# Kernel optimization log

Hardware: AMD Instinct MI355X
Metric: run time of the kernel (lower is better)

## Reference

```python
import jax, jax.numpy as jnp
import numpy as np

DIM = 512
H = 48
W = 48
WS = 6
NH = 16
HEAD = DIM // NH
SCALE = HEAD ** -0.5
MLP_RATIO = 4
EPS = 1e-3  # keras LayerNormalization default epsilon
B = 16
L = H * W
M = WS * WS
NW = (H // WS) * (W // WS)


def _rel_pos_index(ws):
    # replicates tf.meshgrid (indexing='xy') construction exactly
    ch = np.arange(ws)
    cw = np.arange(ws)
    coords = np.stack(np.meshgrid(ch, cw))              # (2, ws, ws)
    cf = coords.reshape(2, -1)                          # (2, M)
    cf1 = np.concatenate([cf, np.zeros((2, 1), cf.dtype)], axis=1)  # (2, M+1) with global (0,0)
    rel = cf[:, :, None] - cf1[:, None, :]              # (2, M, M+1)
    rel = rel.transpose(1, 2, 0).copy()
    rel[:, :, 0] += ws - 1
    rel[:, :, 1] += ws - 1
    rel[:, :, 0] *= 2 * ws - 1
    return rel.sum(-1)                                  # (M, M+1)

REL_IDX = jnp.asarray(_rel_pos_index(WS))


def layernorm(x, g, b):
    m = x.mean(-1, keepdims=True)
    v = ((x - m) ** 2).mean(-1, keepdims=True)
    return (x - m) / jnp.sqrt(v + EPS) * g + b


def setup_inputs() -> dict:
    key = jax.random.key(0)
    ks = jax.random.split(key, 8)
    dense = lambda k, i, o: jax.random.normal(k, (i, o), jnp.float32) * (1.0 / np.sqrt(i))
    return dict(
        x=jax.random.normal(ks[0], (B, L, DIM), jnp.float32),
        xavg=jax.random.normal(ks[1], (B, 1, DIM), jnp.float32),
        w_kv=dense(ks[2], DIM, 2 * DIM), b_kv=jnp.zeros((2 * DIM,), jnp.float32),
        w_q=dense(ks[3], DIM, DIM), b_q=jnp.zeros((DIM,), jnp.float32),
        rel_bias_table=jax.random.normal(ks[4], ((2 * WS - 1) ** 2, NH), jnp.float32) * 0.02,
        g1=jnp.ones((DIM,), jnp.float32), be1=jnp.zeros((DIM,), jnp.float32),
        g2=jnp.ones((DIM,), jnp.float32), be2=jnp.zeros((DIM,), jnp.float32),
        w_fc1=dense(ks[5], DIM, MLP_RATIO * DIM), b_fc1=jnp.zeros((MLP_RATIO * DIM,), jnp.float32),
        w_fc2=dense(ks[6], MLP_RATIO * DIM, DIM), b_fc2=jnp.zeros((DIM,), jnp.float32),
    )


def _heads(t):
    # (B*, N, C) -> (B*, NH, N, HEAD)
    return t.reshape(t.shape[0], t.shape[1], NH, HEAD).transpose(0, 2, 1, 3)


def _forward(x, xavg, w_kv, b_kv, w_q, b_q, rel_bias_table, g1, be1, g2, be2,
             w_fc1, b_fc1, w_fc2, b_fc2):
    shortcut, shortcut_avg = x, xavg
    xn = layernorm(x, g1, be1)                          # (B, L, C)
    xavgn = layernorm(xavg, g1, be1)                    # (B, 1, C)

    # window partition: (B, L, C) -> (B*NW, M, C)
    xw = xn.reshape(B, H // WS, WS, W // WS, WS, DIM)
    xw = xw.transpose(0, 1, 3, 2, 4, 5).reshape(B * NW, M, DIM)

    # per-window tokens + repeated global token as keys/values
    xavgR = jnp.repeat(xavgn, NW, axis=0)               # (B*NW, 1, C), batch-major like tf.repeat
    x_c = jnp.concatenate([xw, xavgR], axis=1)          # (B*NW, M+1, C)

    kv = x_c @ w_kv + b_kv                              # (B*NW, M+1, 2C)
    q = xw @ w_q + b_q                                  # (B*NW, M, C)
    q_avg = xavgn @ w_q + b_q                           # (B, 1, C)
    kv_g = xn @ w_kv + b_kv                             # (B, L, 2C)

    k, v = jnp.split(kv, 2, axis=-1)
    kg, vg = jnp.split(kv_g, 2, axis=-1)

    qh = _heads(q) * SCALE                              # (B*NW, NH, M, HEAD)
    attn = jnp.einsum('bhqd,bhkd->bhqk', qh, _heads(k))  # (B*NW, NH, M, M+1)
    bias = rel_bias_table[REL_IDX.reshape(-1)].reshape(M, M + 1, NH)
    attn = attn + bias.transpose(2, 0, 1)[None]
    attn = jax.nn.softmax(attn, axis=-1)
    xo = jnp.einsum('bhqk,bhkd->bhqd', attn, _heads(v))
    xo = xo.transpose(0, 2, 1, 3).reshape(B * NW, M, DIM)

    # global token attends to all tokens
    qg = _heads(q_avg) * SCALE                          # (B, NH, 1, HEAD)
    attng = jax.nn.softmax(jnp.einsum('bhqd,bhkd->bhqk', qg, _heads(kg)), axis=-1)
    xavg_o = jnp.einsum('bhqk,bhkd->bhqd', attng, _heads(vg))
    xavg_o = xavg_o.transpose(0, 2, 1, 3).reshape(B, 1, DIM)

    # window reverse: (B*NW, M, C) -> (B, L, C)
    xr = xo.reshape(B, H // WS, W // WS, WS, WS, DIM)
    xr = xr.transpose(0, 1, 3, 2, 4, 5).reshape(B, L, DIM)

    x = shortcut + xr
    xavg = shortcut_avg + xavg_o

    mlp = lambda t: jax.nn.gelu(t @ w_fc1 + b_fc1, approximate=False) @ w_fc2 + b_fc2
    x = x + mlp(layernorm(x, g2, be2))
    xavg = xavg + mlp(layernorm(xavg, g2, be2))
    return x, xavg


def reference(x, xavg, w_kv, b_kv, w_q, b_q, rel_bias_table, g1, be1, g2, be2,
              w_fc1, b_fc1, w_fc2, b_fc2):
    return _forward(x, xavg, w_kv, b_kv, w_q, b_q, rel_bias_table, g1, be1, g2, be2,
                    w_fc1, b_fc1, w_fc2, b_fc2)
```

## Files before the change

### kernel.cpp

```cpp
#include <hip/hip_runtime.h>
#include <stdint.h>

#define DIM 512
#define NHEAD 16
#define HEADD 32
#define BATCH 16
#define SEQL 2304
#define XROWS (BATCH*SEQL)
#define NROWS (XROWS + BATCH)
#define ATT_SCALE 0.17677669529663687f

typedef __attribute__((ext_vector_type(8))) short short8;
typedef __attribute__((ext_vector_type(4))) float f32x4;

__device__ __forceinline__ float bf2f(unsigned short v) {
    union { unsigned u; float f; } t; t.u = ((unsigned)v) << 16; return t.f;
}
__device__ __forceinline__ unsigned short f2bf(float f) {
    union { float f; unsigned u; } t; t.f = f;
    unsigned r = t.u + 0x7fffu + ((t.u >> 16) & 1u);
    return (unsigned short)(r >> 16);
}
__device__ __forceinline__ void unpack8(const int4 c, float* o) {
    union { unsigned u; float f; } t;
    unsigned w0 = (unsigned)c.x, w1 = (unsigned)c.y, w2 = (unsigned)c.z, w3 = (unsigned)c.w;
    t.u = w0 << 16;         o[0] = t.f;
    t.u = w0 & 0xffff0000u; o[1] = t.f;
    t.u = w1 << 16;         o[2] = t.f;
    t.u = w1 & 0xffff0000u; o[3] = t.f;
    t.u = w2 << 16;         o[4] = t.f;
    t.u = w2 & 0xffff0000u; o[5] = t.f;
    t.u = w3 << 16;         o[6] = t.f;
    t.u = w3 & 0xffff0000u; o[7] = t.f;
}
__device__ __forceinline__ void gl_lds16(const void* g, void* l) {
    __builtin_amdgcn_global_load_lds((const __attribute__((address_space(1))) unsigned int*)g,
                                     (__attribute__((address_space(3))) unsigned int*)l,
                                     16, 0, 0);
}

__device__ __forceinline__ float gelu_exact(float v) {
    union { float f; unsigned u; } zc; zc.f = v * 0.70710678118654752f;
    unsigned sgn = zc.u & 0x80000000u;
    union { float f; unsigned u; } az; az.u = zc.u & 0x7fffffffu;
    float t  = __builtin_amdgcn_rcpf(fmaf(0.3275911f, az.f, 1.0f));
    float p  = t * fmaf(t, fmaf(t, fmaf(t, fmaf(t, 1.061405429f, -1.453152027f),
                                        1.421413741f), -0.284496736f), 0.254829592f);
    float e  = __expf(-az.f * az.f);
    union { float f; unsigned u; } er; er.f = fmaf(-p, e, 1.0f);
    er.u |= sgn;
    return 0.5f * v * (1.0f + er.f);
}

__device__ __forceinline__ void ln_row(const float* __restrict__ src, int lane,
                                       const float* __restrict__ g, const float* __restrict__ be,
                                       unsigned short* __restrict__ outrow) {
    int c0 = lane * 8;
    float4 v0 = *(const float4*)(src + c0);
    float4 v1 = *(const float4*)(src + c0 + 4);
    float s = v0.x+v0.y+v0.z+v0.w + v1.x+v1.y+v1.z+v1.w;
    float q = v0.x*v0.x+v0.y*v0.y+v0.z*v0.z+v0.w*v0.w + v1.x*v1.x+v1.y*v1.y+v1.z*v1.z+v1.w*v1.w;
    for (int m = 1; m < 64; m <<= 1) { s += __shfl_xor(s, m); q += __shfl_xor(q, m); }
    float mean = s * (1.0f/512.0f);
    float var  = q * (1.0f/512.0f) - mean*mean;
    float rs = rsqrtf(var + 1e-3f);
    float4 g0 = *(const float4*)(g + c0);
    float4 g1 = *(const float4*)(g + c0 + 4);
    float4 b0 = *(const float4*)(be + c0);
    float4 b1 = *(const float4*)(be + c0 + 4);
    unsigned short o[8];
    o[0] = f2bf((v0.x-mean)*rs*g0.x + b0.x);
    o[1] = f2bf((v0.y-mean)*rs*g0.y + b0.y);
    o[2] = f2bf((v0.z-mean)*rs*g0.z + b0.z);
    o[3] = f2bf((v0.w-mean)*rs*g0.w + b0.w);
    o[4] = f2bf((v1.x-mean)*rs*g1.x + b1.x);
    o[5] = f2bf((v1.y-mean)*rs*g1.y + b1.y);
    o[6] = f2bf((v1.z-mean)*rs*g1.z + b1.z);
    o[7] = f2bf((v1.w-mean)*rs*g1.w + b1.w);
    *(int4*)(outrow + c0) = *(const int4*)o;
}

#define TPOSE_BLKS 2816
#define SPACK_BLKS 90
#define LN1_BLKS   9220
__global__ __launch_bounds__(256) void prep_kernel(const float* __restrict__ w_q,
                                                   const float* __restrict__ w_kv,
                                                   const float* __restrict__ w_fc1,
                                                   const float* __restrict__ w_fc2,
                                                   unsigned short* __restrict__ Wqkv_t,
                                                   unsigned short* __restrict__ Wfc1_t,
                                                   unsigned short* __restrict__ Wfc2_t,
                                                   const float* __restrict__ b_q,
                                                   const float* __restrict__ b_kv,
                                                   const float* __restrict__ rel_table,
                                                   float* __restrict__ bqkv,
                                                   float* __restrict__ bias_exp,
                                                   const float* __restrict__ x,
                                                   const float* __restrict__ xavg,
                                                   const float* __restrict__ g1,
                                                   const float* __restrict__ be1,
                                                   unsigned short* __restrict__ xn) {
    __shared__ float tile[32][33];
    int blk = blockIdx.x;
    if (blk < TPOSE_BLKS) {
        int t = blk;
        const float* src; unsigned short* dst;
        int Kd, Nd, rowOff, tk;
        if (t < 256)        { src = w_q;   dst = Wqkv_t; Kd = 512;  Nd = 512;  rowOff = 0;   tk = 16; }
        else if (t < 768)   { t -= 256;  src = w_kv;  dst = Wqkv_t; Kd = 512;  Nd = 1024; rowOff = 512; tk = 16; }
        else if (t < 1792)  { t -= 768;  src = w_fc1; dst = Wfc1_t; Kd = 512;  Nd = 2048; rowOff = 0;   tk = 16; }
        else                { t -= 1792; src = w_fc2; dst = Wfc2_t; Kd = 2048; Nd = 512;  rowOff = 0;   tk = 64; }
        int k0 = (t % tk) * 32;
        int n0 = (t / tk) * 32;
        int tx = threadIdx.x & 31, ty = threadIdx.x >> 5;
        #pragma unroll
        for (int r = 0; r < 32; r += 8)
            tile[r + ty][tx] = src[(long)(k0 + r + ty) * Nd + n0 + tx];
        __syncthreads();
        #pragma unroll
        for (int r = 0; r < 32; r += 8)
            dst[(long)(rowOff + n0 + r + ty) * Kd + k0 + tx] = f2bf(tile[tx][r + ty]);
        return;
    }
    blk -= TPOSE_BLKS;
    if (blk < SPACK_BLKS) {
        int i = blk * 256 + threadIdx.x;
        if (i < 1536) { bqkv[i] = (i < 512) ? b_q[i] : b_kv[i - 512]; return; }
        i -= 1536;
        if (i < NHEAD*36*37) {
            int h = i / (36*37); int rem = i % (36*37); int qi = rem / 37; int j = rem % 37;
            int c0m = qi % 6, c1m = qi / 6;
            int c0n = (j < 36) ? (j % 6) : 0;
            int c1n = (j < 36) ? (j / 6) : 0;
            int id = (c0m - c0n + 5) * 11 + (c1m - c1n + 5);
            bias_exp[i] = rel_table[id * NHEAD + h];
        }
        return;
    }
    blk -= SPACK_BLKS;
    int wv = threadIdx.x >> 6, lane = threadIdx.x & 63;
    int r = blk * 4 + wv;
    if (r >= NROWS) return;
    const float* src = (r < XROWS) ? (x + (long)r * DIM) : (xavg + (long)(r - XROWS) * DIM);
    ln_row(src, lane, g1, be1, xn + (long)r * DIM);
}

__global__ __launch_bounds__(256) void ln_kernel(const float* __restrict__ p1,
                                                 const float* __restrict__ g, const float* __restrict__ be,
                                                 unsigned short* __restrict__ out, int nrows) {
    int wv = threadIdx.x >> 6, lane = threadIdx.x & 63;
    int r = blockIdx.x * 4 + wv;
    if (r >= nrows) return;
    ln_row(p1 + (long)r * DIM, lane, g, be, out + (long)r * DIM);
}

template<bool GELU_ACT, bool OUT_BF16, bool HAS_RES>
__global__ __launch_bounds__(256) void gemm_kernel(const short* __restrict__ A,
                                                   const short* __restrict__ Bt,
                                                   const float* __restrict__ bias,
                                                   void* __restrict__ Cout,
                                                   const float* __restrict__ Res,
                                                   int M, int N, int K, int nbx) {
    __shared__ short lds_a[128 * 64];
    __shared__ short lds_b[128 * 64];
    const int tid = threadIdx.x;
    const int lane = tid & 63;
    const int wv = tid >> 6;

    const int nwg = gridDim.x;
    const int orig = blockIdx.x;
    const int q = nwg >> 3, r = nwg & 7;
    const int xcd = orig & 7, lid = orig >> 3;
    const int wg = (xcd < r ? xcd * (q + 1) : r * (q + 1) + (xcd - r) * q) + lid;
    const int m0 = (wg / nbx) * 128;
    const int n0 = (wg % nbx) * 128;
    const int wm = (wv >> 1) * 64;
    const int wn = (wv & 1) * 64;

    f32x4 acc[4][4];
    #pragma unroll
    for (int i = 0; i < 4; i++)
        #pragma unroll
        for (int j = 0; j < 4; j++) { acc[i][j][0]=0.f; acc[i][j][1]=0.f; acc[i][j][2]=0.f; acc[i][j][3]=0.f; }

    const int srow = tid >> 3;
    const int msl  = (tid & 7) ^ (srow & 7);
    const short* Aa = A + (long)(m0 + srow) * K + msl * 8;
    const short* Bb = Bt + (long)(n0 + srow) * K + msl * 8;
    short* la = lds_a + tid * 8;
    short* lb = lds_b + tid * 8;

    const int quad = lane >> 4;
    const int l15 = lane & 15;
    const short* ra0 = lds_a + (wm + l15) * 64 + ((quad)     ^ (l15 & 7)) * 8;
    const short* ra1 = lds_a + (wm + l15) * 64 + ((4 + quad) ^ (l15 & 7)) * 8;
    const short* rb0 = lds_b + (wn + l15) * 64 + ((quad)     ^ (l15 & 7)) * 8;
    const short* rb1 = lds_b + (wn + l15) * 64 + ((4 + quad) ^ (l15 & 7)) * 8;

    for (int k0 = 0; k0 < K; k0 += 64) {
        __syncthreads();
        #pragma unroll
        for (int i = 0; i < 4; i++) {
            gl_lds16(Aa + (long)(i * 32) * K + k0, la + i * 256 * 8);
            gl_lds16(Bb + (long)(i * 32) * K + k0, lb + i * 256 * 8);
        }
        __syncthreads();
        short8 af[4], bf4[4];
        #pragma unroll
        for (int mt = 0; mt < 4; mt++) af[mt] = *(const short8*)(ra0 + mt * 16 * 64);
        #pragma unroll
        for (int nt = 0; nt < 4; nt++) bf4[nt] = *(const short8*)(rb0 + nt * 16 * 64);
        #pragma unroll
        for (int mt = 0; mt < 4; mt++)
            #pragma unroll
            for (int nt = 0; nt < 4; nt++)
                acc[mt][nt] = __builtin_amdgcn_mfma_f32_16x16x32_bf16(af[mt], bf4[nt], acc[mt][nt], 0, 0, 0);
        #pragma unroll
        for (int mt = 0; mt < 4; mt++) af[mt] = *(const short8*)(ra1 + mt * 16 * 64);
        #pragma unroll
        for (int nt = 0; nt < 4; nt++) bf4[nt] = *(const short8*)(rb1 + nt * 16 * 64);
        #pragma unroll
        for (int mt = 0; mt < 4; mt++)
            #pragma unroll
            for (int nt = 0; nt < 4; nt++)
                acc[mt][nt] = __builtin_amdgcn_mfma_f32_16x16x32_bf16(af[mt], bf4[nt], acc[mt][nt], 0, 0, 0);
    }

    #pragma unroll
    for (int mt = 0; mt < 4; mt++) {
        int rbase = m0 + wm + mt * 16 + quad * 4;
        #pragma unroll
        for (int nt = 0; nt < 4; nt++) {
            int col = n0 + wn + nt * 16 + l15;
            float bv = bias[col];
            #pragma unroll
            for (int r2 = 0; r2 < 4; r2++) {
                int row = rbase + r2;
                if (row < M) {
                    float v = acc[mt][nt][r2] + bv;
                    if (GELU_ACT) v = gelu_exact(v);
                    if (HAS_RES) v += Res[(long)row * N + col];
                    if (OUT_BF16) ((unsigned short*)Cout)[(long)row * N + col] = f2bf(v);
                    else          ((float*)Cout)[(long)row * N + col] = v;
                }
            }
        }
    }
}

__global__ __launch_bounds__(256) void attn_kernel(const short* __restrict__ qkv,
                                                   const float* __restrict__ bias_exp,
                                                   const float* __restrict__ xin,
                                                   const float* __restrict__ xavg,
                                                   float* __restrict__ XALL) {
    __shared__ short vt[4][32 * 64];
    __shared__ short pl[4][48 * 64];
    __shared__ float sums[4][48];
    const int tid = threadIdx.x;
    if (blockIdx.x < 4096) {
        const int wv = tid >> 6;
        const int lane = tid & 63;
        const int gw = blockIdx.x * 4 + wv;
        const int win = gw >> 4;
        const int h = gw & 15;
        const int b = win >> 6;
        const int i1 = (win >> 3) & 7;
        const int i3 = win & 7;
        short* VT = vt[wv];
        short* PL = pl[wv];
        float* SM = sums[wv];
        const int quad = lane >> 4;
        const int l15 = lane & 15;

        {
            int4 z; z.x = 0; z.y = 0; z.z = 0; z.w = 0;
            int4* v4 = (int4*)VT;
            #pragma unroll
            for (int i = 0; i < 4; i++) v4[lane + 64 * i] = z;
            int4* p4 = (int4*)PL;
            #pragma unroll
            for (int i = 0; i < 6; i++) p4[lane + 64 * i] = z;
        }
        for (int c = lane; c < 148; c += 64) {
            int j = c >> 2, dg = c & 3;
            long grow;
            if (j < 36) { int i2 = j / 6, i4 = j % 6; grow = (long)b * SEQL + (i1*6 + i2) * 48 + i3*6 + i4; }
            else grow = XROWS + b;
            int4 raw = *(const int4*)(qkv + grow * 1536 + 1024 + h * 32 + dg * 8);
            const unsigned short* u = (const unsigned short*)&raw;
            #pragma unroll
            for (int t = 0; t < 8; t++) VT[(dg * 8 + t) * 64 + j] = (short)u[t];
        }
        __syncthreads();

        short8 qf[3], kf[3];
        #pragma unroll
        for (int tm = 0; tm < 3; tm++) {
            int qi = tm * 16 + l15;
            if (qi < 36) {
                int i2 = qi / 6, i4 = qi % 6;
                long grow = (long)b * SEQL + (i1*6 + i2) * 48 + i3*6 + i4;
                qf[tm] = *(const short8*)(qkv + grow * 1536 + h * 32 + quad * 8);
            } else {
                #pragma unroll
                for (int i = 0; i < 8; i++) qf[tm][i] = 0;
            }
        }
        #pragma unroll
        for (int tn = 0; tn < 3; tn++) {
            int j = tn * 16 + l15;
            if (j <= 36) {
                long grow;
                if (j < 36) { int i2 = j / 6, i4 = j % 6; grow = (long)b * SEQL + (i1*6 + i2) * 48 + i3*6 + i4; }
                else grow = XROWS + b;
                kf[tn] = *(const short8*)(qkv + grow * 1536 + 512 + h * 32 + quad * 8);
            } else {
                #pragma unroll
                for (int i = 0; i < 8; i++) kf[tn][i] = 0;
            }
        }
        f32x4 s[3][3];
        #pragma unroll
        for (int tm = 0; tm < 3; tm++)
            #pragma unroll
            for (int tn = 0; tn < 3; tn++) {
                f32x4 z; z[0]=0.f; z[1]=0.f; z[2]=0.f; z[3]=0.f;
                s[tm][tn] = __builtin_amdgcn_mfma_f32_16x16x32_bf16(qf[tm], kf[tn], z, 0, 0, 0);
            }
        #pragma unroll
        for (int tm = 0; tm < 3; tm++)
            #pragma unroll
            for (int r = 0; r < 4; r++) {
                int qi = tm * 16 + quad * 4 + r;
                const float* bh = bias_exp + h * (36*37) + (qi < 36 ? qi : 35) * 37;
                #pragma unroll
                for (int tn = 0; tn < 3; tn++) {
                    int j = tn * 16 + l15;
                    float bv = bh[j <= 36 ? j : 36];
                    float v = fmaf(s[tm][tn][r], ATT_SCALE, bv);
                    s[tm][tn][r] = (j <= 36) ? v : -1e30f;
                }
            }
        #pragma unroll
        for (int tm = 0; tm < 3; tm++)
            #pragma unroll
            for (int r = 0; r < 4; r++) {
                float mx = fmaxf(fmaxf(s[tm][0][r], s[tm][1][r]), s[tm][2][r]);
                for (int m = 1; m < 16; m <<= 1) mx = fmaxf(mx, __shfl_xor(mx, m));
                float e0 = __expf(s[tm][0][r] - mx);
                float e1 = __expf(s[tm][1][r] - mx);
                float e2 = __expf(s[tm][2][r] - mx);
                float sum = e0 + e1 + e2;
                for (int m = 1; m < 16; m <<= 1) sum += __shfl_xor(sum, m);
                s[tm][0][r] = e0; s[tm][1][r] = e1; s[tm][2][r] = e2;
                if (l15 == 0) SM[tm * 16 + quad * 4 + r] = 1.0f / sum;
            }
        #pragma unroll
        for (int tm = 0; tm < 3; tm++)
            #pragma unroll
            for (int r = 0; r < 4; r++) {
                int row = (tm * 16 + quad * 4 + r) * 64;
                #pragma unroll
                for (int tn = 0; tn < 3; tn++)
                    PL[row + tn * 16 + l15] = (short)f2bf(s[tm][tn][r]);
            }
        f32x4 o[2][3];
        #pragma unroll
        for (int i = 0; i < 2; i++)
            #pragma unroll
            for (int j = 0; j < 3; j++) { o[i][j][0]=0.f; o[i][j][1]=0.f; o[i][j][2]=0.f; o[i][j][3]=0.f; }
        #pragma unroll
        for (int ch = 0; ch < 2; ch++) {
            short8 va[2], pb[3];
            #pragma unroll
            for (int tmd = 0; tmd < 2; tmd++)
                va[tmd] = *(const short8*)(VT + (tmd * 16 + l15) * 64 + ch * 32 + quad * 8);
            #pragma unroll
            for (int tnq = 0; tnq < 3; tnq++)
                pb[tnq] = *(const short8*)(PL + (tnq * 16 + l15) * 64 + ch * 32 + quad * 8);
            #pragma unroll
            for (int tmd = 0; tmd < 2; tmd++)
                #pragma unroll
                for (int tnq = 0; tnq < 3; tnq++)
                    o[tmd][tnq] = __builtin_amdgcn_mfma_f32_16x16x32_bf16(va[tmd], pb[tnq], o[tmd][tnq], 0, 0, 0);
        }
        #pragma unroll
        for (int tnq = 0; tnq < 3; tnq++) {
            int qi = tnq * 16 + l15;
            if (qi >= 36) continue;
            int i2 = qi / 6, i4 = qi % 6;
            long growq = (long)b * SEQL + (i1*6 + i2) * 48 + i3*6 + i4;
            float is = SM[qi];
            #pragma unroll
            for (int tmd = 0; tmd < 2; tmd++) {
                long base = growq * DIM + h * 32 + tmd * 16 + quad * 4;
                float4 xv = *(const float4*)(xin + base);
                float4 ov;
                ov.x = xv.x + o[tmd][tnq][0] * is;
                ov.y = xv.y + o[tmd][tnq][1] * is;
                ov.z = xv.z + o[tmd][tnq][2] * is;
                ov.w = xv.w + o[tmd][tnq][3] * is;
                *(float4*)(XALL + base) = ov;
            }
        }
        return;
    }
    {
        const int bb = blockIdx.x - 4096;
        const int b = bb >> 4;
        const int h = bb & 15;
        __shared__ float qs[32];
        __shared__ float redm[4], redsum[4];
        __shared__ float wout[4][32];
        if (tid < 32) qs[tid] = bf2f(((const unsigned short*)qkv)[(long)(XROWS + b) * 1536 + h * 32 + tid]);
        __syncthreads();
        float qr[32];
        #pragma unroll
        for (int d = 0; d < 32; d++) qr[d] = qs[d];
        float s[9];
        float mx = -1e30f;
        #pragma unroll
        for (int i = 0; i < 9; i++) {
            int t = tid + i * 256;
            const int4* kp = (const int4*)(qkv + (long)(b * SEQL + t) * 1536 + 512 + h * 32);
            float kr[32];
            unpack8(kp[0], kr); unpack8(kp[1], kr + 8); unpack8(kp[2], kr + 16); unpack8(kp[3], kr + 24);
            float d0 = 0.f, d1 = 0.f, d2 = 0.f, d3 = 0.f;
            #pragma unroll
            for (int dd = 0; dd < 8; dd++) {
                d0 += qr[dd] * kr[dd]; d1 += qr[8+dd] * kr[8+dd];
                d2 += qr[16+dd] * kr[16+dd]; d3 += qr[24+dd] * kr[24+dd];
            }
            s[i] = (d0 + d1 + d2 + d3) * ATT_SCALE;
            mx = fmaxf(mx, s[i]);
        }
        for (int m = 1; m < 64; m <<= 1) mx = fmaxf(mx, __shfl_xor(mx, m));
        if ((tid & 63) == 0) redm[tid >> 6] = mx;
        __syncthreads();
        mx = fmaxf(fmaxf(redm[0], redm[1]), fmaxf(redm[2], redm[3]));
        float sum = 0.f;
        #pragma unroll
        for (int i = 0; i < 9; i++) { s[i] = __expf(s[i] - mx); sum += s[i]; }
        for (int m = 1; m < 64; m <<= 1) sum += __shfl_xor(sum, m);
        if ((tid & 63) == 0) redsum[tid >> 6] = sum;
        __syncthreads();
        sum = redsum[0] + redsum[1] + redsum[2] + redsum[3];
        float o[32];
        #pragma unroll
        for (int d = 0; d < 32; d++) o[d] = 0.f;
        #pragma unroll
        for (int i = 0; i < 9; i++) {
            int t = tid + i * 256;
            const int4* vp = (const int4*)(qkv + (long)(b * SEQL + t) * 1536 + 1024 + h * 32);
            float vr[32];
            unpack8(vp[0], vr); unpack8(vp[1], vr + 8); unpack8(vp[2], vr + 16); unpack8(vp[3], vr + 24);
            float p = s[i];
            #pragma unroll
            for (int d = 0; d < 32; d++) o[d] += p * vr[d];
        }
        for (int m = 1; m < 64; m <<= 1) {
            #pragma unroll
            for (int d = 0; d < 32; d++) o[d] += __shfl_xor(o[d], m);
        }
        if ((tid & 63) == 0) {
            #pragma unroll
            for (int d = 0; d < 32; d++) wout[tid >> 6][d] = o[d];
        }
        __syncthreads();
        if (tid < 32) {
            float t = wout[0][tid] + wout[1][tid] + wout[2][tid] + wout[3][tid];
            XALL[(long)(XROWS + b) * DIM + h * 32 + tid] = xavg[b * DIM + h * 32 + tid] + t / sum;
        }
    }
}

extern "C" void kernel_launch(void* const* d_in, const int* in_sizes, int n_in,
                              void* d_out, int out_size, void* d_ws, size_t ws_size,
                              hipStream_t stream) {
    const float* x      = (const float*)d_in[0];
    const float* xavg   = (const float*)d_in[1];
    const float* w_kv   = (const float*)d_in[2];
    const float* b_kv   = (const float*)d_in[3];
    const float* w_q    = (const float*)d_in[4];
    const float* b_q    = (const float*)d_in[5];
    const float* rel    = (const float*)d_in[6];
    const float* g1     = (const float*)d_in[7];
    const float* be1    = (const float*)d_in[8];
    const float* g2     = (const float*)d_in[9];
    const float* be2    = (const float*)d_in[10];
    const float* w_fc1  = (const float*)d_in[11];
    const float* b_fc1  = (const float*)d_in[12];
    const float* w_fc2  = (const float*)d_in[13];
    const float* b_fc2  = (const float*)d_in[14];

    char* ws = (char*)d_ws;
    size_t off = 0;
    auto alloc = [&](size_t bytes) { void* p = ws + off; off += (bytes + 255) & ~(size_t)255; return p; };
    short* qkv_h          = (short*)alloc((size_t)NROWS * 2048 * 2);
    float* XALL           = (float*)alloc((size_t)NROWS * 512 * 4);
    short* xn             = (short*)alloc((size_t)NROWS * 512 * 2);
    unsigned short* Wqkv_t = (unsigned short*)alloc((size_t)1536 * 512 * 2);
    unsigned short* Wfc1_t = (unsigned short*)alloc((size_t)2048 * 512 * 2);
    unsigned short* Wfc2_t = (unsigned short*)alloc((size_t)512 * 2048 * 2);
    float* bqkv           = (float*)alloc(1536 * 4);
    float* bias_exp       = (float*)alloc((size_t)NHEAD * 36 * 37 * 4);

    const int MB = (NROWS + 127) / 128;

    prep_kernel<<<TPOSE_BLKS + SPACK_BLKS + LN1_BLKS, 256, 0, stream>>>(
        w_q, w_kv, w_fc1, w_fc2, Wqkv_t, Wfc1_t, Wfc2_t,
        b_q, b_kv, rel, bqkv, bias_exp,
        x, xavg, g1, be1, (unsigned short*)xn);
    gemm_kernel<false, true, false><<<12 * MB, 256, 0, stream>>>(
        xn, (const short*)Wqkv_t, bqkv, qkv_h, nullptr, NROWS, 1536, 512, 12);
    attn_kernel<<<4096 + 256, 256, 0, stream>>>(qkv_h, bias_exp, x, xavg, XALL);
    ln_kernel<<<(NROWS + 3) / 4, 256, 0, stream>>>(XALL, g2, be2, (unsigned short*)xn, NROWS);
    gemm_kernel<true, true, false><<<16 * MB, 256, 0, stream>>>(
        xn, (const short*)Wfc1_t, b_fc1, qkv_h, nullptr, NROWS, 2048, 512, 16);
    gemm_kernel<false, false, true><<<4 * MB, 256, 0, stream>>>(
        qkv_h, (const short*)Wfc2_t, b_fc2, d_out, XALL, NROWS, 512, 2048, 4);
}
```

Before: 679.6 us.

## Stage GEMM epilogue through LDS for coalesced vector stores; vectorize V transpose load

The GEMM epilogue now writes the accumulator tile into shared memory one 16-row slice at a time. Each thread then reads 16 contiguous columns and applies bias, GELU and residual before writing with wide vector stores, replacing scattered scalar stores. This is meant to cut uncoalesced global write and residual read traffic, at the cost of extra barriers and LDS round trips. The attention kernel's V transpose now has each lane load a whole 32-element head row with four int4 loads, instead of spreading it over strided iterations.

```diff
diff --git a/kernel.cpp b/kernel.cpp
--- a/kernel.cpp
+++ b/kernel.cpp
@@ -161,8 +161,9 @@
                                                    void* __restrict__ Cout,
                                                    const float* __restrict__ Res,
                                                    int M, int N, int K, int nbx) {
-    __shared__ short lds_a[128 * 64];
-    __shared__ short lds_b[128 * 64];
+    __shared__ short lds[2 * 128 * 64];
+    short* lds_a = lds;
+    short* lds_b = lds + 128 * 64;
     const int tid = threadIdx.x;
     const int lane = tid & 63;
     const int wv = tid >> 6;
@@ -226,22 +227,64 @@
                 acc[mt][nt] = __builtin_amdgcn_mfma_f32_16x16x32_bf16(af[mt], bf4[nt], acc[mt][nt], 0, 0, 0);
     }
 
+    float* ctile = (float*)lds;
+    const int lrow_w = ((wv >> 1) << 4) + quad * 4;
+    const int col_w  = ((wv & 1) << 6) + l15;
+    const int lrow_r = tid >> 3;
+    const int cg     = tid & 7;
+    const int sub    = lrow_r & 15, half = lrow_r >> 4;
+    float bv[16];
+    #pragma unroll
+    for (int i = 0; i < 4; i++)
+        *(float4*)(bv + i * 4) = *(const float4*)(bias + n0 + cg * 16 + i * 4);
+
     #pragma unroll
     for (int mt = 0; mt < 4; mt++) {
-        int rbase = m0 + wm + mt * 16 + quad * 4;
-        #pragma unroll
-        for (int nt = 0; nt < 4; nt++) {
-            int col = n0 + wn + nt * 16 + l15;
-            float bv = bias[col];
-            #pragma unroll
-            for (int r2 = 0; r2 < 4; r2++) {
-                int row = rbase + r2;
-                if (row < M) {
-                    float v = acc[mt][nt][r2] + bv;
-                    if (GELU_ACT) v = gelu_exact(v);
-                    if (HAS_RES) v += Res[(long)row * N + col];
-                    if (OUT_BF16) ((unsigned short*)Cout)[(long)row * N + col] = f2bf(v);
-                    else          ((float*)Cout)[(long)row * N + col] = v;
+        __syncthreads();
+        #pragma unroll
+        for (int nt = 0; nt < 4; nt++)
+            #pragma unroll
+            for (int r2 = 0; r2 < 4; r2++)
+                ctile[(lrow_w + r2) * 132 + col_w + nt * 16] = acc[mt][nt][r2];
+        __syncthreads();
+        int grow = m0 + half * 64 + mt * 16 + sub;
+        if (grow < M) {
+            int gcol = n0 + cg * 16;
+            float v[16];
+            #pragma unroll
+            for (int i = 0; i < 4; i++)
+                *(float4*)(v + i * 4) = *(const float4*)(ctile + lrow_r * 132 + cg * 16 + i * 4);
+            float rv[16];
+            if (HAS_RES) {
+                #pragma unroll
+                for (int i = 0; i < 4; i++)
+                    *(float4*)(rv + i * 4) = *(const float4*)(Res + (long)grow * N + gcol + i * 4);
+            }
+            if (OUT_BF16) {
+                unsigned short ob[16];
+                #pragma unroll
+                for (int i = 0; i < 16; i++) {
+                    float vv = v[i] + bv[i];
+                    if (GELU_ACT) vv = gelu_exact(vv);
+                    if (HAS_RES) vv += rv[i];
+                    ob[i] = f2bf(vv);
+                }
+                unsigned short* dst = (unsigned short*)Cout + (long)grow * N + gcol;
+                *(int4*)dst       = *(const int4*)ob;
+                *(int4*)(dst + 8) = *(const int4*)(ob + 8);
+            } else {
+                float* dst = (float*)Cout + (long)grow * N + gcol;
+                #pragma unroll
+                for (int i = 0; i < 4; i++) {
+                    float4 ov;
+                    float* vp = v + i * 4;
+                    float* rp = rv + i * 4;
+                    ov.x = vp[0] + bv[i*4+0]; ov.y = vp[1] + bv[i*4+1];
+                    ov.z = vp[2] + bv[i*4+2]; ov.w = vp[3] + bv[i*4+3];
+                    if (GELU_ACT) { ov.x = gelu_exact(ov.x); ov.y = gelu_exact(ov.y);
+                                    ov.z = gelu_exact(ov.z); ov.w = gelu_exact(ov.w); }
+                    if (HAS_RES) { ov.x += rp[0]; ov.y += rp[1]; ov.z += rp[2]; ov.w += rp[3]; }
+                    *(float4*)(dst + i * 4) = ov;
                 }
             }
         }
@@ -281,15 +324,24 @@
             #pragma unroll
             for (int i = 0; i < 6; i++) p4[lane + 64 * i] = z;
         }
-        for (int c = lane; c < 148; c += 64) {
-            int j = c >> 2, dg = c & 3;
+        if (lane < 37) {
             long grow;
-            if (j < 36) { int i2 = j / 6, i4 = j % 6; grow = (long)b * SEQL + (i1*6 + i2) * 48 + i3*6 + i4; }
+            if (lane < 36) { int i2 = lane / 6, i4 = lane % 6; grow = (long)b * SEQL + (i1*6 + i2) * 48 + i3*6 + i4; }
             else grow = XROWS + b;
-            int4 raw = *(const int4*)(qkv + grow * 1536 + 1024 + h * 32 + dg * 8);
-            const unsigned short* u = (const unsigned short*)&raw;
-            #pragma unroll
-            for (int t = 0; t < 8; t++) VT[(dg * 8 + t) * 64 + j] = (short)u[t];
+            const int4* vp = (const int4*)(qkv + grow * 1536 + 1024 + h * 32);
+            int4 r0 = vp[0], r1 = vp[1], r2v = vp[2], r3 = vp[3];
+            const unsigned short* u0 = (const unsigned short*)&r0;
+            const unsigned short* u1 = (const unsigned short*)&r1;
+            const unsigned short* u2 = (const unsigned short*)&r2v;
+            const unsigned short* u3 = (const unsigned short*)&r3;
+            #pragma unroll
+            for (int t = 0; t < 8; t++) VT[t * 64 + lane]        = (short)u0[t];
+            #pragma unroll
+            for (int t = 0; t < 8; t++) VT[(8 + t) * 64 + lane]  = (short)u1[t];
+            #pragma unroll
+            for (int t = 0; t < 8; t++) VT[(16 + t) * 64 + lane] = (short)u2[t];
+            #pragma unroll
+            for (int t = 0; t < 8; t++) VT[(24 + t) * 64 + lane] = (short)u3[t];
         }
         __syncthreads();
 
```

New measurement: 677.1 us. About the same (-0.4%).
